# Kernel tuning notes

Measured on AMD Instinct MI355X. Metric: run time of the kernel, lower is better.

Reference implementation:

```python
import jax, jax.numpy as jnp
import numpy as np

B, C, E, H = 8, 2048, 1024, 128


def setup_inputs() -> dict:
    key = jax.random.key(0)
    k1, k2, k3, k4 = jax.random.split(key, 4)
    x = jax.random.normal(k1, (B, C, E), dtype=jnp.float32)
    # store projection weights as (E, H) so projection is x @ W
    Wq = jax.random.normal(k2, (E, H), dtype=jnp.float32) * (E ** -0.5)
    Wk = jax.random.normal(k3, (E, H), dtype=jnp.float32) * (E ** -0.5)
    Wv = jax.random.normal(k4, (E, H), dtype=jnp.float32) * (E ** -0.5)
    return {"x": x, "Wq": Wq, "Wk": Wk, "Wv": Wv}


def reference(x, Wq, Wk, Wv):
    # x: (B, C, E) -> out: (B, C, H)
    _, c, e = x.shape
    q = x @ Wq  # (B, C, H)
    k = x @ Wk  # (B, C, H)
    v = x @ Wv  # (B, C, H)
    # NOTE: original scales by embed_size**0.5, not head_size**0.5
    scale = jnp.asarray(e, x.dtype) ** 0.5
    w = jnp.einsum('bqh,bkh->bqk', q, k) / scale  # (B, C, C)
    causal = jnp.tril(jnp.ones((c, c), dtype=bool))
    w = jnp.where(causal, w, -jnp.inf)
    w = jax.nn.softmax(w, axis=-1)
    # dropout_rate = 0.0 -> identity (eval mode)
    out = w @ v  # (B, C, H)
    return out
```

## Files before the change

### kernel.cpp

```cpp
#include <hip/hip_runtime.h>
#include <hip/hip_bf16.h>
#include <stdint.h>

#define B_ 8
#define C_ 2048
#define E_ 1024
#define H_ 128
#define M_ (B_*C_)
#define SLOTS_B 144

typedef __attribute__((ext_vector_type(8))) short bf16x8;
typedef __attribute__((ext_vector_type(4))) float f32x4;

__device__ __forceinline__ unsigned short f2bf(float f) {
    union { float f; unsigned int u; } v; v.f = f;
    unsigned int u = v.u;
    u += 0x7fff + ((u >> 16) & 1);
    return (unsigned short)(u >> 16);
}
__device__ __forceinline__ float bf2f(unsigned short u) {
    union { unsigned int i; float f; } v; v.i = ((unsigned int)u) << 16; return v.f;
}
__device__ __forceinline__ unsigned int pack2bf(float lo, float hi) {
    union { float f; unsigned int u; } a, b; a.f = lo; b.f = hi;
    return __builtin_amdgcn_perm(b.u + 0x8000u, a.u + 0x8000u, 0x07060302);
}

#define GLOAD_LDS16(g, l) \
    __builtin_amdgcn_global_load_lds((const __attribute__((address_space(1))) void*)(g), \
                                     (__attribute__((address_space(3))) void*)(l), 16, 0, 0)

__global__ __launch_bounds__(256) void wt3_kernel(const float* __restrict__ Wq,
                                                  const float* __restrict__ Wk,
                                                  const float* __restrict__ Wv,
                                                  unsigned short* __restrict__ WT3) {
    int z = blockIdx.y;
    const float* W = (z == 0) ? Wq : (z == 1) ? Wk : Wv;
    unsigned short* o = WT3 + (size_t)z * H_ * E_;
    int g = blockIdx.x * 256 + threadIdx.x;
    int lrow = g & 15;
    int lq   = (g >> 4) & 3;
    int ni   = (g >> 6) & 1;
    int wid  = (g >> 7) & 3;
    int ks   = (g >> 9) & 1;
    int t    = g >> 10;
    int k = t * 64 + ks * 32 + lq * 8;
    int h = wid * 32 + ni * 16 + lrow;
    unsigned short v[8];
#pragma unroll
    for (int j = 0; j < 8; ++j)
        v[j] = f2bf(W[(size_t)(k + j) * H_ + h]);
    *(bf16x8*)&o[(size_t)g * 8] = *(const bf16x8*)v;
}

#define MF(a, b, c) __builtin_amdgcn_mfma_f32_16x16x32_bf16((a), (b), (c), 0, 0, 0)

__global__ __launch_bounds__(256) void proj_kernel(const float* __restrict__ x,
                                                   const unsigned short* __restrict__ WT3,
                                                   unsigned short* __restrict__ QKV) {
    __shared__ __align__(16) float Asf[3][32][64];

    const int tid = threadIdx.x;
    const int wid = tid >> 6, lane = tid & 63;
    const int lrow = lane & 15, lq = lane >> 4;
    const int wcol = wid * 32;
    const int row0 = blockIdx.x * 32;
    const unsigned short* wbase = WT3 + (size_t)wid * 1024 + (size_t)lane * 8;

    const int srow = tid >> 4;
    const int slotL = tid & 15;

    auto ASTAGE = [&](int buf, int t) {
#pragma unroll
        for (int s = 0; s < 2; ++s) {
            int row = s * 16 + srow;
            const float* src = x + (size_t)(row0 + row) * E_ + t * 64
                             + ((slotL ^ (row & 7)) * 4);
            GLOAD_LDS16(src, (char*)&Asf[buf][0][0] + s * 4096 + tid * 16);
        }
    };

    f32x4 acc[3][2][2];
#pragma unroll
    for (int w = 0; w < 3; ++w)
#pragma unroll
        for (int mi = 0; mi < 2; ++mi)
#pragma unroll
            for (int ni = 0; ni < 2; ++ni) acc[w][mi][ni] = (f32x4){0.f, 0.f, 0.f, 0.f};

    ASTAGE(0, 0);
    ASTAGE(1, 1);

    for (int t = 0; t < 16; ++t) {
        const int a0 = t % 3;
        asm volatile("s_waitcnt vmcnt(2)\n\ts_barrier" ::: "memory");
        __builtin_amdgcn_sched_barrier(0);
        if (t < 15) ASTAGE((t + 2) % 3, min(t + 2, 15));

        bf16x8 bw[3][2][2];
        const unsigned short* wp = wbase + (size_t)t * 8192;
#pragma unroll
        for (int w = 0; w < 3; ++w)
#pragma unroll
            for (int ks = 0; ks < 2; ++ks)
#pragma unroll
                for (int ni = 0; ni < 2; ++ni)
                    bw[w][ks][ni] = *(const bf16x8*)(wp + (size_t)w * 131072 + ks * 4096 + ni * 512);

        bf16x8 af[2][2];
#pragma unroll
        for (int mi = 0; mi < 2; ++mi)
#pragma unroll
            for (int ks = 0; ks < 2; ++ks) {
                int row = mi * 16 + lrow;
                int m7 = row & 7;
                int s0 = 2 * (ks * 4 + lq);
                f32x4 f0 = *(const f32x4*)&Asf[a0][row][((s0)     ^ m7) * 4];
                f32x4 f1 = *(const f32x4*)&Asf[a0][row][((s0 + 1) ^ m7) * 4];
                union { unsigned int u[4]; bf16x8 v; } pk;
                pk.u[0] = pack2bf(f0[0], f0[1]);
                pk.u[1] = pack2bf(f0[2], f0[3]);
                pk.u[2] = pack2bf(f1[0], f1[1]);
                pk.u[3] = pack2bf(f1[2], f1[3]);
                af[mi][ks] = pk.v;
            }

        __builtin_amdgcn_s_setprio(1);
#pragma unroll
        for (int ks = 0; ks < 2; ++ks)
#pragma unroll
            for (int w = 0; w < 3; ++w)
#pragma unroll
                for (int ni = 0; ni < 2; ++ni)
#pragma unroll
                    for (int mi = 0; mi < 2; ++mi)
                        acc[w][mi][ni] = MF(af[mi][ks], bw[w][ks][ni], acc[w][mi][ni]);
        __builtin_amdgcn_s_setprio(0);
    }

#pragma unroll
    for (int w = 0; w < 2; ++w) {
        const float qs = (w == 0) ? 0.03125f : 1.0f;
        unsigned short* outp = QKV + (size_t)w * M_ * H_;
#pragma unroll
        for (int mi = 0; mi < 2; ++mi) {
            int r0 = row0 + mi * 16 + lq * 4;
#pragma unroll
            for (int ni = 0; ni < 2; ++ni) {
                int col = wcol + ni * 16 + lrow;
#pragma unroll
                for (int r = 0; r < 4; ++r)
                    outp[(size_t)(r0 + r) * H_ + col] = f2bf(acc[w][mi][ni][r] * qs);
            }
        }
    }
    {
        unsigned short* vt = QKV + (size_t)2 * M_ * H_;
        int b = row0 / C_;
        int cbase = row0 % C_;
#pragma unroll
        for (int mi = 0; mi < 2; ++mi) {
            int c0 = cbase + mi * 16 + lq * 4;
#pragma unroll
            for (int ni = 0; ni < 2; ++ni) {
                int h = wcol + ni * 16 + lrow;
                __align__(8) unsigned short p[4] = {f2bf(acc[2][mi][ni][0]), f2bf(acc[2][mi][ni][1]),
                                                    f2bf(acc[2][mi][ni][2]), f2bf(acc[2][mi][ni][3])};
                *(uint2*)&vt[((size_t)b * H_ + h) * C_ + c0] = *(const uint2*)p;
            }
        }
    }
}

__global__ __launch_bounds__(256) void attn_kernel(const unsigned short* __restrict__ QKV,
                                                   unsigned short* __restrict__ PO,
                                                   float* __restrict__ ML,
                                                   float* __restrict__ out) {
    __shared__ __align__(16) unsigned short Ks[2][64][128];
    __shared__ __align__(16) unsigned short Vt[2][128][64];

    const unsigned short* Q  = QKV;
    const unsigned short* K  = QKV + (size_t)M_ * H_;
    const unsigned short* VT = QKV + (size_t)2 * M_ * H_;

    const int tid = threadIdx.x, wid = tid >> 6, lane = tid & 63;
    const int lrow = lane & 15, lq = lane >> 4, lk = lq * 8;
    const int b = blockIdx.x;
    const int rr = blockIdx.y;

    int j = 0;
#pragma unroll
    for (int jj = 1; jj < 32; ++jj) {
        int q = jj >> 2, s = jj & 3;
        if (jj + 2 * q * (q - 1) + s * q <= rr) j = jj;
    }
    const int qj = j >> 2, sj = j & 3;
    const int Cj = j + 2 * qj * (qj - 1) + sj * qj;
    const int c = rr - Cj;
    const int nch = qj + 1;
    const int t0 = c * 4;
    const int t1 = min(t0 + 4, j + 1);

    const int q0w = j * 64 + wid * 16;
    const unsigned short* Kb  = K  + (size_t)b * C_ * H_;
    const unsigned short* VTb = VT + (size_t)b * H_ * C_;
    const int qabs = q0w + lrow;

    const int krow = tid >> 4, kg = tid & 15;
    const int vrow = tid >> 3, vg = tid & 7;

    bf16x8 qf[4];
#pragma unroll
    for (int kf = 0; kf < 4; ++kf)
        qf[kf] = *(const bf16x8*)&Q[((size_t)b * C_ + q0w + lrow) * H_ + kf * 32 + lk];

    f32x4 o[8];
#pragma unroll
    for (int nf = 0; nf < 8; ++nf) o[nf] = (f32x4){0.f, 0.f, 0.f, 0.f};
    float m = -INFINITY, l = 0.f;

    auto STAGE = [&](int buf, int t) {
        const int kv0 = t * 64;
#pragma unroll
        for (int s = 0; s < 4; ++s) {
            int r = s * 16 + krow;
            int prow = ((r & 0x10) << 1) | ((r & 0x0C) << 1) | ((r & 0x20) >> 3) | (r & 3);
            GLOAD_LDS16(&Kb[(size_t)(kv0 + prow) * H_ + ((kg ^ (r & 15)) * 8)],
                        (char*)&Ks[buf][0][0] + s * 4096 + tid * 16);
        }
#pragma unroll
        for (int s = 0; s < 4; ++s) {
            int h = s * 32 + vrow;
            GLOAD_LDS16(&VTb[(size_t)h * C_ + kv0 + ((vg ^ (h & 7)) * 8)],
                        (char*)&Vt[buf][0][0] + s * 4096 + tid * 16);
        }
    };

    STAGE(0, t0);

    for (int t = t0; t < t1; ++t) {
        const int cur = (t - t0) & 1;
        __syncthreads();
        if (t + 1 < t1) STAGE(cur ^ 1, t + 1);

        const int kv0 = t * 64;
        f32x4 s[4];
        __builtin_amdgcn_s_setprio(1);
#pragma unroll
        for (int nf = 0; nf < 4; ++nf) {
            s[nf] = (f32x4){0.f, 0.f, 0.f, 0.f};
            const int rk = nf * 16 + lrow;
#pragma unroll
            for (int kf = 0; kf < 4; ++kf) {
                bf16x8 kb = *(const bf16x8*)&Ks[cur][rk][((kf * 4 + lq) ^ (rk & 15)) * 8];
                s[nf] = __builtin_amdgcn_mfma_f32_16x16x32_bf16(kb, qf[kf], s[nf], 0, 0, 0);
            }
        }
        __builtin_amdgcn_s_setprio(0);
        bf16x8 vb[8][2];
#pragma unroll
        for (int nf = 0; nf < 8; ++nf) {
            const int h = nf * 16 + lrow;
#pragma unroll
            for (int kf2 = 0; kf2 < 2; ++kf2)
                vb[nf][kf2] = *(const bf16x8*)&Vt[cur][h][((kf2 * 4 + lq) ^ (h & 7)) * 8];
        }

        if (t == j) {
#pragma unroll
            for (int nf = 0; nf < 4; ++nf) {
                int kvb = kv0 + ((nf & 1) << 5) + (lq << 3) + ((nf >> 1) << 2);
#pragma unroll
                for (int r = 0; r < 4; ++r)
                    if (kvb + r > qabs) s[nf][r] = -INFINITY;
            }
        }
        float mt = s[0][0];
#pragma unroll
        for (int nf = 0; nf < 4; ++nf)
#pragma unroll
            for (int r = 0; r < 4; ++r) mt = fmaxf(mt, s[nf][r]);
        mt = fmaxf(mt, __shfl_xor(mt, 16));
        mt = fmaxf(mt, __shfl_xor(mt, 32));

        float mn = fmaxf(m, mt);
        float corr = __expf(m - mn);
        m = mn;

        float p[4][4];
        float ps = 0.f;
#pragma unroll
        for (int nf = 0; nf < 4; ++nf)
#pragma unroll
            for (int r = 0; r < 4; ++r) {
                float e = __expf(s[nf][r] - mn);
                p[nf][r] = e;
                ps += e;
            }
        ps += __shfl_xor(ps, 16);
        ps += __shfl_xor(ps, 32);
        l = l * corr + ps;

        float corr4[4];
#pragma unroll
        for (int r = 0; r < 4; ++r)
            corr4[r] = __shfl(corr, (lane & 48) | (lq * 4 + r));
#pragma unroll
        for (int nf = 0; nf < 8; ++nf)
#pragma unroll
            for (int r = 0; r < 4; ++r) o[nf][r] *= corr4[r];

        bf16x8 pa[2];
#pragma unroll
        for (int kf2 = 0; kf2 < 2; ++kf2) {
            union { unsigned int u[4]; bf16x8 v; } pk;
            pk.u[0] = pack2bf(p[kf2][0],     p[kf2][1]);
            pk.u[1] = pack2bf(p[kf2][2],     p[kf2][3]);
            pk.u[2] = pack2bf(p[kf2 + 2][0], p[kf2 + 2][1]);
            pk.u[3] = pack2bf(p[kf2 + 2][2], p[kf2 + 2][3]);
            pa[kf2] = pk.v;
        }
        __builtin_amdgcn_s_setprio(1);
#pragma unroll
        for (int nf = 0; nf < 8; ++nf)
#pragma unroll
            for (int kf2 = 0; kf2 < 2; ++kf2)
                o[nf] = __builtin_amdgcn_mfma_f32_16x16x32_bf16(pa[kf2], vb[nf][kf2], o[nf], 0, 0, 0);
        __builtin_amdgcn_s_setprio(0);
    }

    float l4[4], m4[4];
#pragma unroll
    for (int r = 0; r < 4; ++r) {
        l4[r] = __shfl(l, (lane & 48) | (lq * 4 + r));
        m4[r] = __shfl(m, (lane & 48) | (lq * 4 + r));
    }
    const int qrow0 = q0w + lq * 4;

    if (nch == 1) {
#pragma unroll
        for (int nf = 0; nf < 8; ++nf) {
            int col = nf * 16 + lrow;
#pragma unroll
            for (int r = 0; r < 4; ++r)
                out[((size_t)b * C_ + qrow0 + r) * H_ + col] = o[nf][r] / l4[r];
        }
    } else {
        const int slot = b * SLOTS_B + rr;
        unsigned short* po = PO + (size_t)slot * 64 * 128;
        const int rl0 = wid * 16 + lq * 4;
#pragma unroll
        for (int nf = 0; nf < 8; ++nf) {
            int col = nf * 16 + lrow;
#pragma unroll
            for (int r = 0; r < 4; ++r)
                po[(size_t)(rl0 + r) * 128 + col] = f2bf(o[nf][r]);
        }
        if (lrow == 0) {
            float* ml = ML + (size_t)slot * 128;
#pragma unroll
            for (int r = 0; r < 4; ++r) {
                ml[rl0 + r] = m4[r];
                ml[64 + rl0 + r] = l4[r];
            }
        }
    }
}

__global__ __launch_bounds__(256) void combine_kernel(const unsigned short* __restrict__ PO,
                                                      const float* __restrict__ ML,
                                                      float* __restrict__ out) {
    const int j = blockIdx.x + 4;
    const int b = blockIdx.y;
    const int q = j >> 2, s = j & 3;
    const int Cj = j + 2 * q * (q - 1) + s * q;
    const int nch = q + 1;
    const int base = b * SLOTS_B + Cj;
    const int row = threadIdx.x >> 2;
    const int colg = (threadIdx.x & 3) * 32;

    float mstar = -INFINITY;
    for (int c = 0; c < nch; ++c)
        mstar = fmaxf(mstar, ML[(size_t)(base + c) * 128 + row]);

    float denom = 0.f;
    float acc[32];
#pragma unroll
    for (int i = 0; i < 32; ++i) acc[i] = 0.f;

    for (int c = 0; c < nch; ++c) {
        float mc = ML[(size_t)(base + c) * 128 + row];
        float lc = ML[(size_t)(base + c) * 128 + 64 + row];
        float w = __expf(mc - mstar);
        denom += w * lc;
        const unsigned short* p = PO + (size_t)(base + c) * 64 * 128 + (size_t)row * 128 + colg;
#pragma unroll
        for (int k = 0; k < 4; ++k) {
            bf16x8 v = *(const bf16x8*)&p[k * 8];
#pragma unroll
            for (int e = 0; e < 8; ++e)
                acc[k * 8 + e] += w * bf2f(((unsigned short*)&v)[e]);
        }
    }
    float inv = 1.f / denom;
    float* op = out + ((size_t)b * C_ + j * 64 + row) * H_ + colg;
#pragma unroll
    for (int k = 0; k < 8; ++k) {
        float4 st = {acc[k * 4] * inv, acc[k * 4 + 1] * inv, acc[k * 4 + 2] * inv, acc[k * 4 + 3] * inv};
        *(float4*)&op[k * 4] = st;
    }
}

extern "C" void kernel_launch(void* const* d_in, const int* in_sizes, int n_in,
                              void* d_out, int out_size, void* d_ws, size_t ws_size,
                              hipStream_t stream) {
    const float* x  = (const float*)d_in[0];
    const float* Wq = (const float*)d_in[1];
    const float* Wk = (const float*)d_in[2];
    const float* Wv = (const float*)d_in[3];
    float* out = (float*)d_out;

    unsigned short* WT3 = (unsigned short*)d_ws;
    unsigned short* QKV = WT3 + (size_t)3 * H_ * E_;
    unsigned short* PO  = QKV + (size_t)3 * M_ * H_;
    float*          ML  = (float*)(PO + (size_t)8 * SLOTS_B * 64 * 128);

    wt3_kernel<<<dim3(64, 3), 256, 0, stream>>>(Wq, Wk, Wv, WT3);
    proj_kernel<<<dim3(M_ / 32), 256, 0, stream>>>(x, WT3, QKV);
    attn_kernel<<<dim3(B_, SLOTS_B), 256, 0, stream>>>(QKV, PO, ML, out);
    combine_kernel<<<dim3(28, B_), 256, 0, stream>>>(PO, ML, out);
}
```

Before: 71.02 us.

## Fully unroll projection K-loop with separate LDS buffers and nontemporal x loads

```diff
diff --git a/kernel.cpp b/kernel.cpp
--- a/kernel.cpp
+++ b/kernel.cpp
@@ -29,6 +29,9 @@
 #define GLOAD_LDS16(g, l) \
     __builtin_amdgcn_global_load_lds((const __attribute__((address_space(1))) void*)(g), \
                                      (__attribute__((address_space(3))) void*)(l), 16, 0, 0)
+#define GLOAD_LDS16_NT(g, l) \
+    __builtin_amdgcn_global_load_lds((const __attribute__((address_space(1))) void*)(g), \
+                                     (__attribute__((address_space(3))) void*)(l), 16, 0, 2)
 
 __global__ __launch_bounds__(256) void wt3_kernel(const float* __restrict__ Wq,
                                                   const float* __restrict__ Wk,
@@ -55,10 +58,54 @@
 
 #define MF(a, b, c) __builtin_amdgcn_mfma_f32_16x16x32_bf16((a), (b), (c), 0, 0, 0)
 
+#define ASTAGE(ARR, T) { \
+    _Pragma("unroll") for (int s_ = 0; s_ < 2; ++s_) { \
+        int row_ = s_ * 16 + srow; \
+        const float* src_ = x + (size_t)(row0 + row_) * E_ + (T) * 64 \
+                          + ((slotL ^ (row_ & 7)) * 4); \
+        GLOAD_LDS16_NT(src_, (char*)&ARR[0][0] + s_ * 4096 + tid * 16); } }
+
+#define BODY(T, AR, AP, PF) { \
+    __builtin_amdgcn_s_barrier(); \
+    __builtin_amdgcn_sched_barrier(0); \
+    bf16x8 bw[3][2][2]; \
+    { const unsigned short* wp_ = wbase + (size_t)(T) * 8192; \
+      _Pragma("unroll") for (int w_ = 0; w_ < 3; ++w_) \
+      _Pragma("unroll") for (int ks_ = 0; ks_ < 2; ++ks_) \
+      _Pragma("unroll") for (int ni_ = 0; ni_ < 2; ++ni_) \
+          bw[w_][ks_][ni_] = *(const bf16x8*)(wp_ + (size_t)w_ * 131072 + ks_ * 4096 + ni_ * 512); } \
+    __builtin_amdgcn_sched_barrier(0); \
+    bf16x8 af[2][2]; \
+    _Pragma("unroll") for (int mi_ = 0; mi_ < 2; ++mi_) \
+    _Pragma("unroll") for (int ks_ = 0; ks_ < 2; ++ks_) { \
+        int row_ = mi_ * 16 + lrow; \
+        int m7_ = row_ & 7; \
+        int s0_ = 2 * (ks_ * 4 + lq); \
+        f32x4 f0_ = *(const f32x4*)&AR[row_][((s0_)     ^ m7_) * 4]; \
+        f32x4 f1_ = *(const f32x4*)&AR[row_][((s0_ + 1) ^ m7_) * 4]; \
+        union { unsigned int u[4]; bf16x8 v; } pk_; \
+        pk_.u[0] = pack2bf(f0_[0], f0_[1]); \
+        pk_.u[1] = pack2bf(f0_[2], f0_[3]); \
+        pk_.u[2] = pack2bf(f1_[0], f1_[1]); \
+        pk_.u[3] = pack2bf(f1_[2], f1_[3]); \
+        af[mi_][ks_] = pk_.v; } \
+    __builtin_amdgcn_sched_barrier(0); \
+    if (PF) ASTAGE(AP, (T) + 2); \
+    __builtin_amdgcn_sched_barrier(0); \
+    __builtin_amdgcn_s_setprio(1); \
+    _Pragma("unroll") for (int ks_ = 0; ks_ < 2; ++ks_) \
+    _Pragma("unroll") for (int w_ = 0; w_ < 3; ++w_) \
+    _Pragma("unroll") for (int ni_ = 0; ni_ < 2; ++ni_) \
+    _Pragma("unroll") for (int mi_ = 0; mi_ < 2; ++mi_) \
+        acc[w_][mi_][ni_] = MF(af[mi_][ks_], bw[w_][ks_][ni_], acc[w_][mi_][ni_]); \
+    __builtin_amdgcn_s_setprio(0); }
+
 __global__ __launch_bounds__(256) void proj_kernel(const float* __restrict__ x,
                                                    const unsigned short* __restrict__ WT3,
                                                    unsigned short* __restrict__ QKV) {
-    __shared__ __align__(16) float Asf[3][32][64];
+    __shared__ __align__(16) float Asf0[32][64];
+    __shared__ __align__(16) float Asf1[32][64];
+    __shared__ __align__(16) float Asf2[32][64];
 
     const int tid = threadIdx.x;
     const int wid = tid >> 6, lane = tid & 63;
@@ -70,16 +117,6 @@
     const int srow = tid >> 4;
     const int slotL = tid & 15;
 
-    auto ASTAGE = [&](int buf, int t) {
-#pragma unroll
-        for (int s = 0; s < 2; ++s) {
-            int row = s * 16 + srow;
-            const float* src = x + (size_t)(row0 + row) * E_ + t * 64
-                             + ((slotL ^ (row & 7)) * 4);
-            GLOAD_LDS16(src, (char*)&Asf[buf][0][0] + s * 4096 + tid * 16);
-        }
-    };
-
     f32x4 acc[3][2][2];
 #pragma unroll
     for (int w = 0; w < 3; ++w)
@@ -88,55 +125,15 @@
 #pragma unroll
             for (int ni = 0; ni < 2; ++ni) acc[w][mi][ni] = (f32x4){0.f, 0.f, 0.f, 0.f};
 
-    ASTAGE(0, 0);
-    ASTAGE(1, 1);
-
-    for (int t = 0; t < 16; ++t) {
-        const int a0 = t % 3;
-        asm volatile("s_waitcnt vmcnt(2)\n\ts_barrier" ::: "memory");
-        __builtin_amdgcn_sched_barrier(0);
-        if (t < 15) ASTAGE((t + 2) % 3, min(t + 2, 15));
-
-        bf16x8 bw[3][2][2];
-        const unsigned short* wp = wbase + (size_t)t * 8192;
-#pragma unroll
-        for (int w = 0; w < 3; ++w)
-#pragma unroll
-            for (int ks = 0; ks < 2; ++ks)
-#pragma unroll
-                for (int ni = 0; ni < 2; ++ni)
-                    bw[w][ks][ni] = *(const bf16x8*)(wp + (size_t)w * 131072 + ks * 4096 + ni * 512);
-
-        bf16x8 af[2][2];
-#pragma unroll
-        for (int mi = 0; mi < 2; ++mi)
-#pragma unroll
-            for (int ks = 0; ks < 2; ++ks) {
-                int row = mi * 16 + lrow;
-                int m7 = row & 7;
-                int s0 = 2 * (ks * 4 + lq);
-                f32x4 f0 = *(const f32x4*)&Asf[a0][row][((s0)     ^ m7) * 4];
-                f32x4 f1 = *(const f32x4*)&Asf[a0][row][((s0 + 1) ^ m7) * 4];
-                union { unsigned int u[4]; bf16x8 v; } pk;
-                pk.u[0] = pack2bf(f0[0], f0[1]);
-                pk.u[1] = pack2bf(f0[2], f0[3]);
-                pk.u[2] = pack2bf(f1[0], f1[1]);
-                pk.u[3] = pack2bf(f1[2], f1[3]);
-                af[mi][ks] = pk.v;
-            }
-
-        __builtin_amdgcn_s_setprio(1);
-#pragma unroll
-        for (int ks = 0; ks < 2; ++ks)
-#pragma unroll
-            for (int w = 0; w < 3; ++w)
-#pragma unroll
-                for (int ni = 0; ni < 2; ++ni)
-#pragma unroll
-                    for (int mi = 0; mi < 2; ++mi)
-                        acc[w][mi][ni] = MF(af[mi][ks], bw[w][ks][ni], acc[w][mi][ni]);
-        __builtin_amdgcn_s_setprio(0);
-    }
+    ASTAGE(Asf0, 0);
+    ASTAGE(Asf1, 1);
+
+    BODY(0,  Asf0, Asf2, 1)  BODY(1,  Asf1, Asf0, 1)  BODY(2,  Asf2, Asf1, 1)
+    BODY(3,  Asf0, Asf2, 1)  BODY(4,  Asf1, Asf0, 1)  BODY(5,  Asf2, Asf1, 1)
+    BODY(6,  Asf0, Asf2, 1)  BODY(7,  Asf1, Asf0, 1)  BODY(8,  Asf2, Asf1, 1)
+    BODY(9,  Asf0, Asf2, 1)  BODY(10, Asf1, Asf0, 1)  BODY(11, Asf2, Asf1, 1)
+    BODY(12, Asf0, Asf2, 1)  BODY(13, Asf1, Asf0, 1)
+    BODY(14, Asf2, Asf1, 0)  BODY(15, Asf0, Asf1, 0)
 
 #pragma unroll
     for (int w = 0; w < 2; ++w) {
```

Result: slower. 78.00 us (+9.8%).
